# Kernel tuning notes

Measured on AMD Instinct MI355X. Metric: run time of the kernel, lower is better.

The kernel has to match this reference:

```python
import jax, jax.numpy as jnp
import numpy as np

B, S, V, E, H, NL, DFF = 16, 16, 64, 64, 8, 4, 2048
L = S * V
DH = E // H
NUM_GRIDS = 100
POI_DIM = 8
OV_DIM = 8


def setup_inputs() -> dict:
    key = jax.random.key(0)
    ks = jax.random.split(key, 32)
    sc = 0.05
    inp = {}
    inp['features'] = jax.random.normal(ks[0], (B, S, V, 3), jnp.float32)
    inp['overlap_tag'] = jax.random.randint(ks[1], (B, S, V), 0, 3)
    inp['poi_id'] = jax.random.randint(ks[2], (B, S, V), 0, NUM_GRIDS + 1)
    # embedders
    inp['W_raw'] = jax.random.normal(ks[3], (3, E), jnp.float32) * sc
    inp['b_raw'] = jnp.zeros((E,), jnp.float32)
    inp['pos_tab'] = jax.random.normal(ks[4], (S, E), jnp.float32) * sc
    inp['type_tab'] = jax.random.normal(ks[5], (V, E), jnp.float32) * sc
    inp['poi_tab'] = jax.random.normal(ks[6], (NUM_GRIDS + 1, POI_DIM), jnp.float32) * sc
    inp['overlap_tab'] = jax.random.normal(ks[7], (3, OV_DIM), jnp.float32) * sc
    inp['W_comb'] = jax.random.normal(ks[8], (E + OV_DIM + POI_DIM, E), jnp.float32) * sc
    inp['b_comb'] = jnp.zeros((E,), jnp.float32)
    # transformer layers (stacked over NL)
    inp['Wqkv'] = jax.random.normal(ks[9], (NL, E, 3 * E), jnp.float32) * sc
    inp['bqkv'] = jnp.zeros((NL, 3 * E), jnp.float32)
    inp['Wo'] = jax.random.normal(ks[10], (NL, E, E), jnp.float32) * sc
    inp['bo'] = jnp.zeros((NL, E), jnp.float32)
    inp['ln1_s'] = jnp.ones((NL, E), jnp.float32)
    inp['ln1_b'] = jnp.zeros((NL, E), jnp.float32)
    inp['W1'] = jax.random.normal(ks[11], (NL, E, DFF), jnp.float32) * sc
    inp['b1'] = jnp.zeros((NL, DFF), jnp.float32)
    inp['W2'] = jax.random.normal(ks[12], (NL, DFF, E), jnp.float32) * sc
    inp['b2'] = jnp.zeros((NL, E), jnp.float32)
    inp['ln2_s'] = jnp.ones((NL, E), jnp.float32)
    inp['ln2_b'] = jnp.zeros((NL, E), jnp.float32)
    inp['W_head'] = jax.random.normal(ks[13], (E, 3), jnp.float32) * sc
    inp['b_head'] = jnp.zeros((3,), jnp.float32)
    return inp


def _layer_norm(x, s, b):
    m = x.mean(-1, keepdims=True)
    v = ((x - m) ** 2).mean(-1, keepdims=True)
    return (x - m) / jnp.sqrt(v + 1e-5) * s + b


def _forward(features, overlap_tag, poi_id, W_raw, b_raw, pos_tab, type_tab,
             poi_tab, overlap_tab, W_comb, b_comb, Wqkv, bqkv, Wo, bo,
             ln1_s, ln1_b, W1, b1, W2, b2, ln2_s, ln2_b, W_head, b_head):
    # padding_idx=0 rows are zero (as in nn.Embedding(padding_idx=0))
    poi_tab = poi_tab.at[0].set(0.0)
    overlap_tab = overlap_tab.at[0].set(0.0)

    zero_mask = (features.sum(-1) == 0).reshape(B, L)  # [B, L]
    ov_idx = jnp.maximum(overlap_tag, 0)
    poi_idx = jnp.maximum(poi_id, 0)

    feat_e = features @ W_raw + b_raw                    # [B,S,V,E]
    concat = jnp.concatenate([feat_e, overlap_tab[ov_idx], poi_tab[poi_idx]], axis=-1)
    x = (concat @ W_comb + b_comb).reshape(B, L, E)      # [B,L,E]

    t_idx = jnp.repeat(jnp.arange(S), V)                 # [L]
    v_idx = jnp.tile(jnp.arange(V), S)                   # [L]
    struct_mask = (t_idx[:, None] != t_idx[None, :]) & (v_idx[:, None] != v_idx[None, :])
    full_mask = struct_mask[None] | zero_mask[:, None, :] | zero_mask[:, :, None]  # [B,L,L]
    bias = jnp.where(full_mask, -jnp.inf, 0.0)[:, None, :, :]  # [B,1,L,L]

    x = x + pos_tab[t_idx][None] + type_tab[v_idx][None]

    scale = 1.0 / jnp.sqrt(jnp.asarray(DH, x.dtype))
    for l in range(NL):
        qkv = x @ Wqkv[l] + bqkv[l]                      # [B,L,3E]
        q, k, v = jnp.split(qkv, 3, axis=-1)
        q = q.reshape(B, L, H, DH)
        k = k.reshape(B, L, H, DH)
        v = v.reshape(B, L, H, DH)
        scores = jnp.einsum('bqhd,bkhd->bhqk', q, k) * scale + bias
        attn = jax.nn.softmax(scores, axis=-1)
        o = jnp.einsum('bhqk,bkhd->bqhd', attn, v).reshape(B, L, E)
        x = _layer_norm(x + o @ Wo[l] + bo[l], ln1_s[l], ln1_b[l])
        ff = jax.nn.relu(x @ W1[l] + b1[l]) @ W2[l] + b2[l]
        x = _layer_norm(x + ff, ln2_s[l], ln2_b[l])

    last = x.reshape(B, S, V, E)[:, -1]                  # [B,V,E]
    return last @ W_head + b_head                        # [B,V,3]


def reference(features, overlap_tag, poi_id, W_raw, b_raw, pos_tab, type_tab,
              poi_tab, overlap_tab, W_comb, b_comb, Wqkv, bqkv, Wo, bo,
              ln1_s, ln1_b, W1, b1, W2, b2, ln2_s, ln2_b, W_head, b_head):
    return _forward(features, overlap_tag, poi_id, W_raw, b_raw, pos_tab, type_tab,
                    poi_tab, overlap_tab, W_comb, b_comb, Wqkv, bqkv, Wo, bo,
                    ln1_s, ln1_b, W1, b1, W2, b2, ln2_s, ln2_b, W_head, b_head)
```

## Files before the change

kernel.cpp:

```cpp
#include <hip/hip_runtime.h>
#include <math.h>

#define BB 16
#define SS 16
#define VVV 64
#define EE 64
#define HHH 8
#define NLAYER 4
#define DFF_ 2048
#define LL 1024
#define BL 16384
#define PERL 131072

typedef __attribute__((ext_vector_type(8))) _Float16 half8;
typedef __attribute__((ext_vector_type(4))) _Float16 half4v;
typedef __attribute__((ext_vector_type(2))) _Float16 half2v;
typedef __attribute__((ext_vector_type(4))) float f32x4;

#if defined(__has_builtin)
#if __has_builtin(__builtin_amdgcn_fdot2)
#define HAVE_FDOT2 1
#endif
#endif

#define SW64(m, k)  (((m) << 6) + ((((k) >> 3) ^ ((m) & 7)) << 3) + ((k) & 7))


__device__ __forceinline__ void ffn_load2(
    const _Float16* __restrict__ w1f, const _Float16* __restrict__ w2f, int g,
    half8 (&a1)[2][2], half8 (&b2w)[2][2], int wn, int lane)
{
  const _Float16* w1t_ = w1f + (size_t)g * 4096;
  const _Float16* w2t_ = w2f + (size_t)g * 4096;
#pragma unroll
  for (int ht = 0; ht < 2; ht++)
#pragma unroll
    for (int ks = 0; ks < 2; ks++)
      a1[ht][ks] = *(const half8*)&w1t_[(size_t)(((wn * 2 + ht) * 2 + ks) * 512) +
                                        lane * 8];
#pragma unroll
  for (int nt = 0; nt < 2; nt++)
#pragma unroll
    for (int ks = 0; ks < 2; ks++)
      b2w[nt][ks] = *(const half8*)&w2t_[(size_t)(((wn * 2 + nt) * 2 + ks) * 512) +
                                         lane * 8];
}

__device__ __forceinline__ void ffn_step2(
    const half8 (&a1)[2][2], const half8 (&b2w)[2][2], const half8 (&xb)[2][2],
    _Float16* hsbuf, const float* __restrict__ b1, int g, f32x4 (&acc)[2][2],
    int wn, int lane)
{
  int quad = lane >> 4, l15 = lane & 15;
  f32x4 hacc[2][2];
#pragma unroll
  for (int ht = 0; ht < 2; ht++)
#pragma unroll
    for (int mt = 0; mt < 2; mt++) hacc[ht][mt] = (f32x4){0.f, 0.f, 0.f, 0.f};
#pragma unroll
  for (int ks = 0; ks < 2; ks++)
#pragma unroll
    for (int ht = 0; ht < 2; ht++)
#pragma unroll
      for (int mt = 0; mt < 2; mt++)
        hacc[ht][mt] = __builtin_amdgcn_mfma_f32_16x16x32_f16(
            a1[ht][ks], xb[mt][ks], hacc[ht][mt], 0, 0, 0);
#pragma unroll
  for (int ht = 0; ht < 2; ht++) {
    float4 bb = *(const float4*)&b1[g * 64 + wn * 32 + ht * 16 + quad * 4];
#pragma unroll
    for (int mt = 0; mt < 2; mt++) {
      f32x4 hv = hacc[ht][mt];
      half4v hp = (half4v){
          (_Float16)fmaxf(hv[0] + bb.x, 0.f), (_Float16)fmaxf(hv[1] + bb.y, 0.f),
          (_Float16)fmaxf(hv[2] + bb.z, 0.f), (_Float16)fmaxf(hv[3] + bb.w, 0.f)};
      *(half4v*)&hsbuf[SW64(mt * 16 + l15, wn * 32 + ht * 16 + quad * 4)] = hp;
    }
  }
  __syncthreads();
#pragma unroll
  for (int ks = 0; ks < 2; ks++)
#pragma unroll
    for (int mt = 0; mt < 2; mt++) {
      half8 a2 = *(const half8*)&hsbuf[SW64(mt * 16 + l15, ks * 32 + quad * 8)];
#pragma unroll
      for (int nt = 0; nt < 2; nt++)
        acc[mt][nt] = __builtin_amdgcn_mfma_f32_16x16x32_f16(a2, b2w[nt][ks],
                                                             acc[mt][nt], 0, 0, 0);
    }
}

__global__ __launch_bounds__(256) void k_prepemb(
    const float* __restrict__ W1, const float* __restrict__ W2,
    const float* __restrict__ Wqkv, const float* __restrict__ Wo,
    const float* __restrict__ Wcomb,
    _Float16* __restrict__ w1f, _Float16* __restrict__ w2f,
    _Float16* __restrict__ wqkvf, _Float16* __restrict__ wof,
    const float* __restrict__ features, const int* __restrict__ ovtag,
    const int* __restrict__ poiid, const float* __restrict__ W_raw,
    const float* __restrict__ b_raw, const float* __restrict__ ov_tab,
    const float* __restrict__ poi_tab, const float* __restrict__ b_comb,
    const float* __restrict__ pos_tab, const float* __restrict__ type_tab,
    _Float16* __restrict__ x1h, float* __restrict__ zm,
    const float* __restrict__ bqkv, _Float16* __restrict__ qbuf,
    _Float16* __restrict__ kbuf, _Float16* __restrict__ vbuf)
{
  int gbx = blockIdx.x;
  int tid = threadIdx.x;

  if (gbx < 272) {
    __shared__ float t[64 * 65];
    int bx = gbx;
    int cc = tid & 63, rr = tid >> 6;
    const float* src; _Float16* dst; int astr;
    if (bx < 128) {
      int l = bx >> 5, g = bx & 31;
      src = W1 + (size_t)l * PERL + g * 64; astr = 2048;
      dst = w1f + (size_t)(l * 32 + g) * 4096;
    } else if (bx < 256) {
      int j = bx - 128; int l = j >> 5, g = j & 31;
      src = W2 + (size_t)l * PERL + (size_t)g * 64 * 64; astr = 64;
      dst = w2f + (size_t)(l * 32 + g) * 4096;
    } else if (bx < 268) {
      int j = bx - 256; int l = j / 3, g = j % 3;
      src = Wqkv + (size_t)l * 64 * 192 + g * 64; astr = 192;
      dst = wqkvf + (size_t)(l * 3 + g) * 4096;
    } else {
      int l = bx - 268;
      src = Wo + (size_t)l * 4096; astr = 64;
      dst = wof + (size_t)l * 4096;
    }
#pragma unroll
    for (int i = 0; i < 16; i++) {
      int a = i * 4 + rr;
      t[cc * 65 + a] = src[(size_t)a * astr + cc];
    }
    __syncthreads();
#pragma unroll
    for (int it = 0; it < 2; it++) {
      int c = tid + it * 256;
      int frag = c >> 6, lane = c & 63;
      int m = (frag >> 1) * 16 + (lane & 15);
      int k0 = (frag & 1) * 32 + (lane >> 4) * 8;
      const float* tr = &t[m * 65 + k0];
      half8 h;
#pragma unroll
      for (int j = 0; j < 8; j++) h[j] = (_Float16)tr[j];
      *(half8*)&dst[(size_t)c * 8] = h;
    }
    return;
  }

  constexpr int KP = 104;
  __shared__ _Float16 As[64 * KP];
  __shared__ _Float16 Bs[64 * KP];
  __shared__ _Float16 xs[4096];
  int raw = gbx - 272;
  int bx = ((raw & 7) << 5) + (raw >> 3);
  int m0 = bx * 64;
  int wave = tid >> 6, lane = tid & 63, quad = lane >> 4, l15 = lane & 15;
  int wm = wave >> 1, wn = wave & 1;
  for (int p = tid; p < 1536; p += 256) {
    int r = p / 24, s = p - r * 24; int c = s * 4;
    int row = m0 + r;
    float f0 = features[row * 3 + 0];
    float f1 = features[row * 3 + 1];
    float f2 = features[row * 3 + 2];
    if (s == 0) zm[row] = ((f0 + f1 + f2) == 0.f) ? 1.f : 0.f;
    half4v h;
#pragma unroll
    for (int j = 0; j < 4; j++) {
      int cc = c + j; float v;
      if (cc < 64) {
        v = b_raw[cc] + f0 * W_raw[cc] + f1 * W_raw[64 + cc] + f2 * W_raw[128 + cc];
      } else if (cc < 72) {
        int tt = ovtag[row]; v = (tt <= 0) ? 0.f : ov_tab[tt * 8 + cc - 64];
      } else if (cc < 80) {
        int tt = poiid[row]; v = (tt <= 0) ? 0.f : poi_tab[tt * 8 + cc - 72];
      } else v = 0.f;
      h[j] = (_Float16)v;
    }
    *(half4v*)&As[r * KP + c] = h;
  }
  for (int p = tid; p < 1536; p += 256) {
    int r = p / 24, s = p - r * 24; int c = s * 4;
    half4v h = (half4v){0, 0, 0, 0};
#pragma unroll
    for (int j = 0; j < 4; j++)
      if (c + j < 80) h[j] = (_Float16)Wcomb[(size_t)(c + j) * 64 + r];
    *(half4v*)&Bs[r * KP + c] = h;
  }
  __syncthreads();
  f32x4 acc[2][2];
#pragma unroll
  for (int mt = 0; mt < 2; mt++)
#pragma unroll
    for (int nt = 0; nt < 2; nt++) {
      float bv = b_comb[wn * 32 + nt * 16 + l15];
      acc[mt][nt] = (f32x4){bv, bv, bv, bv};
    }
#pragma unroll
  for (int ks = 0; ks < 3; ks++) {
    half8 af[2], bf[2];
#pragma unroll
    for (int mt = 0; mt < 2; mt++)
      af[mt] = *(const half8*)&As[(wm * 32 + mt * 16 + l15) * KP + ks * 32 + quad * 8];
#pragma unroll
    for (int nt = 0; nt < 2; nt++)
      bf[nt] = *(const half8*)&Bs[(wn * 32 + nt * 16 + l15) * KP + ks * 32 + quad * 8];
#pragma unroll
    for (int mt = 0; mt < 2; mt++)
#pragma unroll
      for (int nt = 0; nt < 2; nt++)
        acc[mt][nt] = __builtin_amdgcn_mfma_f32_16x16x32_f16(af[mt], bf[nt],
                                                             acc[mt][nt], 0, 0, 0);
  }
#pragma unroll
  for (int mt = 0; mt < 2; mt++)
#pragma unroll
    for (int nt = 0; nt < 2; nt++)
#pragma unroll
      for (int r = 0; r < 4; r++) {
        int lrow = wm * 32 + mt * 16 + quad * 4 + r;
        int row = m0 + lrow;
        int col = wn * 32 + nt * 16 + l15;
        int l = row & (LL - 1);
        float v = acc[mt][nt][r] +
            pos_tab[(l >> 6) * 64 + col] + type_tab[(l & 63) * 64 + col];
        x1h[(size_t)row * 64 + col] = (_Float16)v;
        xs[SW64(lrow, col)] = (_Float16)v;
      }
  __syncthreads();
  half8 af[2][2];
#pragma unroll
  for (int mt = 0; mt < 2; mt++)
#pragma unroll
    for (int ks = 0; ks < 2; ks++)
      af[mt][ks] = *(const half8*)&xs[SW64(wm * 32 + mt * 16 + l15,
                                           ks * 32 + quad * 8)];
#pragma unroll
  for (int nb = 0; nb < 3; nb++) {
    half8 bf[2][2];
#pragma unroll
    for (int nt = 0; nt < 2; nt++)
#pragma unroll
      for (int ks = 0; ks < 2; ks++) {
        int n = nb * 64 + (wn * 2 + nt) * 16 + l15;
#pragma unroll
        for (int j = 0; j < 8; j++)
          bf[nt][ks][j] =
              (_Float16)Wqkv[(size_t)(ks * 32 + quad * 8 + j) * 192 + n];
      }
    f32x4 qacc[2][2];
#pragma unroll
    for (int mt = 0; mt < 2; mt++)
#pragma unroll
      for (int nt = 0; nt < 2; nt++) {
        float bv = bqkv[nb * 64 + wn * 32 + nt * 16 + l15];
        qacc[mt][nt] = (f32x4){bv, bv, bv, bv};
      }
#pragma unroll
    for (int ks = 0; ks < 2; ks++)
#pragma unroll
      for (int mt = 0; mt < 2; mt++)
#pragma unroll
        for (int nt = 0; nt < 2; nt++)
          qacc[mt][nt] = __builtin_amdgcn_mfma_f32_16x16x32_f16(
              af[mt][ks], bf[nt][ks], qacc[mt][nt], 0, 0, 0);
    _Float16* dst = (nb == 0) ? qbuf : ((nb == 1) ? kbuf : vbuf);
#pragma unroll
    for (int mt = 0; mt < 2; mt++)
#pragma unroll
      for (int nt = 0; nt < 2; nt++) {
        int col = wn * 32 + nt * 16 + l15;
        int h = col >> 3, d = col & 7;
#pragma unroll
        for (int r = 0; r < 4; r++) {
          int row = m0 + wm * 32 + mt * 16 + quad * 4 + r;
          int b = row >> 10, rb = row & 1023;
          dst[((size_t)(b * 8 + h) * 1024 + rb) * 8 + d] = (_Float16)qacc[mt][nt][r];
        }
      }
  }
}

__global__ __launch_bounds__(256, 2) void k_layerf(
    const _Float16* __restrict__ qin, const _Float16* __restrict__ kin,
    const _Float16* __restrict__ vin, const float* __restrict__ zm,
    const _Float16* __restrict__ wof, const float* __restrict__ bo,
    _Float16* __restrict__ x1h,
    const float* __restrict__ ln1_s, const float* __restrict__ ln1_b,
    const _Float16* __restrict__ w1f, const _Float16* __restrict__ w2f,
    const float* __restrict__ b1, const float* __restrict__ b2,
    const float* __restrict__ ln2_s, const float* __restrict__ ln2_b,
    const _Float16* __restrict__ wqkvf, const float* __restrict__ bqkv,
    _Float16* __restrict__ qout, _Float16* __restrict__ kout,
    _Float16* __restrict__ vout, int doqkv,
    const float* __restrict__ Wh, const float* __restrict__ bh,
    float* __restrict__ out)
{
  __shared__ float ots[32 * 68];
  __shared__ __align__(16) _Float16 xs[2048];
  __shared__ float x2f[2048];
  __shared__ __align__(16) _Float16 hs[4][2048];
  __shared__ __align__(16) _Float16 os[2048];
  __shared__ float zsh[1024];
  __shared__ __align__(16) _Float16 kvs[8192];
  __shared__ float ots2[32 * 68];
  int tid = threadIdx.x;
  int raw = blockIdx.x;
  int bx = ((raw & 7) << 6) + (raw >> 3);
  int r0 = bx * 32;
  int rb0 = r0 & 1023;
  int wave = tid >> 6, lane = tid & 63;
  int quad = lane >> 4, l15 = lane & 15;
  int grp = wave >> 1, wn = wave & 1;
  int b = r0 >> 10;
  int tq0 = rb0 >> 6;

  for (int p = tid; p < 1024; p += 256)
    zsh[p] = (zm[b * LL + p] != 0.f) ? -20000.f : 0.f;
  for (int p = tid; p < 512; p += 256) {
    int h = p >> 6, row = p & 63;
    size_t gidx = ((size_t)(b * 8 + h) * 1024 + tq0 * 64 + row) * 8;
    *(half8*)&kvs[h * 512 + row * 8] = *(const half8*)&kin[gidx];
    *(half8*)&kvs[4096 + h * 512 + row * 8] = *(const half8*)&vin[gidx];
  }

  half8 obf[2][2];
#pragma unroll
  for (int nt = 0; nt < 2; nt++)
#pragma unroll
    for (int ks = 0; ks < 2; ks++)
      obf[nt][ks] = *(const half8*)&wof[(size_t)(((wn * 2 + nt) * 2 + ks) * 512) +
                                        lane * 8];
  float x1pre[8];
#pragma unroll
  for (int i = 0; i < 8; i++)
    x1pre[i] = (float)x1h[(size_t)(r0 + wave * 8 + i) * 64 + lane];
  float ln1sv = ln1_s[lane], ln1bv = ln1_b[lane];
  float ln2sv = ln2_s[lane], ln2bv = ln2_b[lane];
  half8 a1x[2][2], b2x[2][2], a1y[2][2], b2y[2][2];
  ffn_load2(w1f, w2f, grp, a1x, b2x, wn, lane);
  __syncthreads();

  {
    int lr = tid & 31, hh = tid >> 5;
    int rb = rb0 + lr;
    int vq = rb & 63;
    const _Float16* kb = kin + (size_t)(b * 8 + hh) * 8192;
    const _Float16* vb = vin + (size_t)(b * 8 + hh) * 8192;
    half8 qh = *(const half8*)&qin[(size_t)(b * 8 + hh) * 8192 + (size_t)rb * 8];
    const float scale = 0.3535533905932738f;
    float m = -10000.f, lsum = 0.f;
    float acc[8] = {0.f, 0.f, 0.f, 0.f, 0.f, 0.f, 0.f, 0.f};
    bool zmq = (zsh[rb] < -1.f);

    auto dot = [&](half8 kk) -> float {
      float s = 0.f;
#ifdef HAVE_FDOT2
#pragma unroll
      for (int j = 0; j < 4; j++) {
        half2v qa = (half2v){qh[2 * j], qh[2 * j + 1]};
        half2v ka = (half2v){kk[2 * j], kk[2 * j + 1]};
        s = __builtin_amdgcn_fdot2(qa, ka, s, false);
      }
#else
#pragma unroll
      for (int j = 0; j < 8; j++) s += (float)qh[j] * (float)kk[j];
#endif
      return s;
    };
    auto update = [&](float s, half8 vv) {
      float nm = fmaxf(m, s);
      float r = __expf(m - nm);
      float p = __expf(s - nm);
      lsum = lsum * r + p;
#pragma unroll
      for (int d = 0; d < 8; d++) acc[d] = acc[d] * r + p * (float)vv[d];
      m = nm;
    };

    if (!zmq) {
      for (int base = 0; base < 64; base += 4) {
        half8 kk[4], vv[4]; float sv[4];
#pragma unroll
        for (int j = 0; j < 4; j++) {
          kk[j] = *(const half8*)&kvs[hh * 512 + (base + j) * 8];
          vv[j] = *(const half8*)&kvs[4096 + hh * 512 + (base + j) * 8];
        }
#pragma unroll
        for (int j = 0; j < 4; j++)
          sv[j] = dot(kk[j]) * scale + zsh[tq0 * 64 + base + j];
#pragma unroll
        for (int j = 0; j < 4; j++) update(sv[j], vv[j]);
      }
      for (int bb = 0; bb < 5; bb++) {
        half8 kk[3], vv[3]; float sv[3];
#pragma unroll
        for (int j = 0; j < 3; j++) {
          int cc = bb * 3 + j;
          int tt = cc + ((cc >= tq0) ? 1 : 0);
          int k = tt * 64 + vq;
          kk[j] = *(const half8*)&kb[(size_t)k * 8];
          vv[j] = *(const half8*)&vb[(size_t)k * 8];
          sv[j] = zsh[k];
        }
#pragma unroll
        for (int j = 0; j < 3; j++) sv[j] += dot(kk[j]) * scale;
#pragma unroll
        for (int j = 0; j < 3; j++) update(sv[j], vv[j]);
      }
    }
    float inv = (lsum > 0.f) ? 1.f / lsum : 0.f;
    half8 o;
#pragma unroll
    for (int d = 0; d < 8; d++) o[d] = (_Float16)(acc[d] * inv);
    *(half8*)&os[SW64(lr, hh * 8)] = o;
  }
  __syncthreads();

  {
    half8 af[2];
#pragma unroll
    for (int ks = 0; ks < 2; ks++)
      af[ks] = *(const half8*)&os[SW64(grp * 16 + l15, ks * 32 + quad * 8)];
    f32x4 acc[2];
#pragma unroll
    for (int nt = 0; nt < 2; nt++) {
      float bv = bo[wn * 32 + nt * 16 + l15];
      acc[nt] = (f32x4){bv, bv, bv, bv};
    }
#pragma unroll
    for (int ks = 0; ks < 2; ks++)
#pragma unroll
      for (int nt = 0; nt < 2; nt++)
        acc[nt] = __builtin_amdgcn_mfma_f32_16x16x32_f16(af[ks], obf[nt][ks],
                                                         acc[nt], 0, 0, 0);
#pragma unroll
    for (int nt = 0; nt < 2; nt++)
#pragma unroll
      for (int r = 0; r < 4; r++)
        ots[(grp * 16 + quad * 4 + r) * 68 + wn * 32 + nt * 16 + l15] = acc[nt][r];
  }
  __syncthreads();
  for (int i = 0; i < 8; i++) {
    int row = wave * 8 + i;
    float val = ots[row * 68 + lane] + x1pre[i];
    float sum = val;
#pragma unroll
    for (int o = 32; o > 0; o >>= 1) sum += __shfl_xor(sum, o);
    float mean = sum * (1.f / 64.f);
    float d = val - mean;
    float sq = d * d;
#pragma unroll
    for (int o = 32; o > 0; o >>= 1) sq += __shfl_xor(sq, o);
    float xv = d * rsqrtf(sq * (1.f / 64.f) + 1e-5f) * ln1sv + ln1bv;
    x2f[row * 64 + lane] = xv;
    xs[SW64(row, lane)] = (_Float16)xv;
  }
  __syncthreads();

  half8 xb[2][2];
#pragma unroll
  for (int mt = 0; mt < 2; mt++)
#pragma unroll
    for (int ks = 0; ks < 2; ks++)
      xb[mt][ks] = *(const half8*)&xs[SW64(mt * 16 + l15, ks * 32 + quad * 8)];
  f32x4 acc[2][2];
#pragma unroll
  for (int mt = 0; mt < 2; mt++)
#pragma unroll
    for (int nt = 0; nt < 2; nt++) {
      float bv = (grp == 0) ? b2[wn * 32 + nt * 16 + l15] : 0.f;
      acc[mt][nt] = (f32x4){bv, bv, bv, bv};
    }
  for (int ii = 0; ii < 8; ii++) {
    ffn_load2(w1f, w2f, ii * 4 + 2 + grp, a1y, b2y, wn, lane);
    ffn_step2(a1x, b2x, xb, &hs[grp][0], b1, ii * 4 + grp, acc, wn, lane);
    if (ii < 7) ffn_load2(w1f, w2f, ii * 4 + 4 + grp, a1x, b2x, wn, lane);
    ffn_step2(a1y, b2y, xb, &hs[grp + 2][0], b1, ii * 4 + 2 + grp, acc, wn, lane);
  }
  __syncthreads();
  if (grp == 0) {
#pragma unroll
    for (int mt = 0; mt < 2; mt++)
#pragma unroll
      for (int nt = 0; nt < 2; nt++)
#pragma unroll
        for (int r = 0; r < 4; r++)
          ots[(mt * 16 + quad * 4 + r) * 68 + wn * 32 + nt * 16 + l15] =
              acc[mt][nt][r];
  }
  __syncthreads();
  if (grp == 1) {
#pragma unroll
    for (int mt = 0; mt < 2; mt++)
#pragma unroll
      for (int nt = 0; nt < 2; nt++)
#pragma unroll
        for (int r = 0; r < 4; r++)
          ots[(mt * 16 + quad * 4 + r) * 68 + wn * 32 + nt * 16 + l15] +=
              acc[mt][nt][r];
  }
  __syncthreads();
  for (int i = 0; i < 8; i++) {
    int row = wave * 8 + i;
    size_t off = (size_t)(r0 + row) * 64 + lane;
    float val = ots[row * 68 + lane] + x2f[row * 64 + lane];
    float sum = val;
#pragma unroll
    for (int o = 32; o > 0; o >>= 1) sum += __shfl_xor(sum, o);
    float mean = sum * (1.f / 64.f);
    float d = val - mean;
    float sq = d * d;
#pragma unroll
    for (int o = 32; o > 0; o >>= 1) sq += __shfl_xor(sq, o);
    float xv = d * rsqrtf(sq * (1.f / 64.f) + 1e-5f) * ln2sv + ln2bv;
    if (doqkv) x1h[off] = (_Float16)xv;
    x2f[row * 64 + lane] = xv;
    xs[SW64(row, lane)] = (_Float16)xv;
  }
  if (!doqkv) {
    __syncthreads();
    if ((bx & 31) >= 30 && tid < 96) {
      int bb2 = bx >> 5;
      int i = tid / 3, j = tid - i * 3;
      int vglob = (bx & 1) * 32 + i;
      float a = bh[j];
      for (int e = 0; e < 64; e++)
        a += x2f[i * 64 + e] * Wh[e * 3 + j];
      out[((size_t)(bb2 * 64 + vglob)) * 3 + j] = a;
    }
    return;
  }
  __syncthreads();
  half8 af[2][2];
#pragma unroll
  for (int mt = 0; mt < 2; mt++)
#pragma unroll
    for (int ks = 0; ks < 2; ks++)
      af[mt][ks] = *(const half8*)&xs[SW64(mt * 16 + l15, ks * 32 + quad * 8)];
  for (int nb = 0; nb < 3; nb++) {
    const _Float16* bt = wqkvf + (size_t)nb * 4096;
    half8 bf[2];
#pragma unroll
    for (int ks = 0; ks < 2; ks++)
      bf[ks] = *(const half8*)&bt[(size_t)((wave * 2 + ks) * 512) + lane * 8];
    f32x4 qacc[2];
#pragma unroll
    for (int mt = 0; mt < 2; mt++) {
      float bv = bqkv[nb * 64 + wave * 16 + l15];
      qacc[mt] = (f32x4){bv, bv, bv, bv};
    }
#pragma unroll
    for (int ks = 0; ks < 2; ks++)
#pragma unroll
      for (int mt = 0; mt < 2; mt++)
        qacc[mt] = __builtin_amdgcn_mfma_f32_16x16x32_f16(af[mt][ks], bf[ks],
                                                          qacc[mt], 0, 0, 0);
    _Float16* dst = (nb == 0) ? qout : ((nb == 1) ? kout : vout);
    int col = wave * 16 + l15;
    int h2 = col >> 3, d2 = col & 7;
#pragma unroll
    for (int mt = 0; mt < 2; mt++)
#pragma unroll
      for (int r = 0; r < 4; r++) {
        int row = r0 + mt * 16 + quad * 4 + r;
        int rbq = row & 1023;
        dst[((size_t)(b * 8 + h2) * 1024 + rbq) * 8 + d2] = (_Float16)qacc[mt][r];
      }
  }
}

extern "C" void kernel_launch(void* const* d_in, const int* in_sizes, int n_in,
                              void* d_out, int out_size, void* d_ws, size_t ws_size,
                              hipStream_t stream) {
  const float* features = (const float*)d_in[0];
  const int*   ovtag    = (const int*)d_in[1];
  const int*   poiid    = (const int*)d_in[2];
  const float* W_raw    = (const float*)d_in[3];
  const float* b_raw    = (const float*)d_in[4];
  const float* pos_tab  = (const float*)d_in[5];
  const float* type_tab = (const float*)d_in[6];
  const float* poi_tab  = (const float*)d_in[7];
  const float* ov_tab   = (const float*)d_in[8];
  const float* W_comb   = (const float*)d_in[9];
  const float* b_comb   = (const float*)d_in[10];
  const float* Wqkv     = (const float*)d_in[11];
  const float* bqkv     = (const float*)d_in[12];
  const float* Wo       = (const float*)d_in[13];
  const float* bo       = (const float*)d_in[14];
  const float* ln1_s    = (const float*)d_in[15];
  const float* ln1_b    = (const float*)d_in[16];
  const float* W1       = (const float*)d_in[17];
  const float* b1       = (const float*)d_in[18];
  const float* W2       = (const float*)d_in[19];
  const float* b2       = (const float*)d_in[20];
  const float* ln2_s    = (const float*)d_in[21];
  const float* ln2_b    = (const float*)d_in[22];
  const float* W_head   = (const float*)d_in[23];
  const float* b_head   = (const float*)d_in[24];
  float* out = (float*)d_out;
  float* ws  = (float*)d_ws;

  float* zm  = ws;
  _Float16* x1h = (_Float16*)(zm + BL);
  _Float16* qbA = x1h + (size_t)BL * 64;
  _Float16* kbA = qbA + (size_t)BL * 64;
  _Float16* vbA = kbA + (size_t)BL * 64;
  _Float16* qbB = vbA + (size_t)BL * 64;
  _Float16* kbB = qbB + (size_t)BL * 64;
  _Float16* vbB = kbB + (size_t)BL * 64;
  _Float16* w1f    = vbB + (size_t)BL * 64;
  _Float16* w2f    = w1f + (size_t)NLAYER * PERL;
  _Float16* wqkvf  = w2f + (size_t)NLAYER * PERL;
  _Float16* wof    = wqkvf + (size_t)NLAYER * 3 * 4096;

  k_prepemb<<<528, 256, 0, stream>>>(W1, W2, Wqkv, Wo, W_comb,
                                     w1f, w2f, wqkvf, wof,
                                     features, ovtag, poiid, W_raw, b_raw,
                                     ov_tab, poi_tab, b_comb, pos_tab, type_tab,
                                     x1h, zm, bqkv, qbA, kbA, vbA);
  for (int l = 0; l < NLAYER; l++) {
    const _Float16* qin = (l & 1) ? qbB : qbA;
    const _Float16* kin = (l & 1) ? kbB : kbA;
    const _Float16* vin = (l & 1) ? vbB : vbA;
    _Float16* qout = (l & 1) ? qbA : qbB;
    _Float16* kout = (l & 1) ? kbA : kbB;
    _Float16* vout = (l & 1) ? vbA : vbB;
    int doqkv = (l < NLAYER - 1);
    k_layerf<<<512, 256, 0, stream>>>(
        qin, kin, vin, zm,
        wof + (size_t)l * 4096, bo + l * EE, x1h,
        ln1_s + l * EE, ln1_b + l * EE,
        w1f + (size_t)l * PERL, w2f + (size_t)l * PERL,
        b1 + l * DFF_, b2 + l * EE,
        ln2_s + l * EE, ln2_b + l * EE,
        wqkvf + (size_t)(l + 1 < NLAYER ? l + 1 : 0) * 3 * 4096,
        bqkv + (l + 1 < NLAYER ? l + 1 : 0) * 192,
        qout, kout, vout, doqkv, W_head, b_head, out);
  }
}
```

Before: 273.5 us.

## Process 64 rows per block with 512 threads to halve FFN weight traffic

Each layer block now covers 64 rows (a full time step of vertices) with 8 waves instead of 32 rows with 4 waves, launching 256 blocks instead of 512. Each streamed W1/W2 chunk is applied to twice as many rows, so per-row weight traffic drops, and the K/V tile of the current time step is shared across all its vertices. The shared buffers are packed into one aliased 126 KB array, and FFN partial sums are reduced through two buffers across four wave groups. In exchange only one block fits per CU, the grid shrinks to 256 blocks, and register pressure rises from the larger accumulator tiles.

```diff
diff --git a/kernel.cpp b/kernel.cpp
--- a/kernel.cpp
+++ b/kernel.cpp
@@ -25,7 +25,6 @@
 
 #define SW64(m, k)  (((m) << 6) + ((((k) >> 3) ^ ((m) & 7)) << 3) + ((k) & 7))
 
-
 __device__ __forceinline__ void ffn_load2(
     const _Float16* __restrict__ w1f, const _Float16* __restrict__ w2f, int g,
     half8 (&a1)[2][2], half8 (&b2w)[2][2], int wn, int lane)
@@ -46,31 +45,27 @@
                                          lane * 8];
 }
 
-__device__ __forceinline__ void ffn_step2(
-    const half8 (&a1)[2][2], const half8 (&b2w)[2][2], const half8 (&xb)[2][2],
-    _Float16* hsbuf, const float* __restrict__ b1, int g, f32x4 (&acc)[2][2],
+__device__ __forceinline__ void ffn_step4(
+    const half8 (&a1)[2][2], const half8 (&b2w)[2][2], const half8 (&xb)[4][2],
+    _Float16* hsbuf, const float* __restrict__ b1, int g, f32x4 (&acc)[4][2],
     int wn, int lane)
 {
   int quad = lane >> 4, l15 = lane & 15;
-  f32x4 hacc[2][2];
-#pragma unroll
-  for (int ht = 0; ht < 2; ht++)
-#pragma unroll
-    for (int mt = 0; mt < 2; mt++) hacc[ht][mt] = (f32x4){0.f, 0.f, 0.f, 0.f};
-#pragma unroll
-  for (int ks = 0; ks < 2; ks++)
-#pragma unroll
-    for (int ht = 0; ht < 2; ht++)
-#pragma unroll
-      for (int mt = 0; mt < 2; mt++)
-        hacc[ht][mt] = __builtin_amdgcn_mfma_f32_16x16x32_f16(
-            a1[ht][ks], xb[mt][ks], hacc[ht][mt], 0, 0, 0);
 #pragma unroll
   for (int ht = 0; ht < 2; ht++) {
+    f32x4 hacc[4];
+#pragma unroll
+    for (int mt = 0; mt < 4; mt++) hacc[mt] = (f32x4){0.f, 0.f, 0.f, 0.f};
+#pragma unroll
+    for (int ks = 0; ks < 2; ks++)
+#pragma unroll
+      for (int mt = 0; mt < 4; mt++)
+        hacc[mt] = __builtin_amdgcn_mfma_f32_16x16x32_f16(
+            a1[ht][ks], xb[mt][ks], hacc[mt], 0, 0, 0);
     float4 bb = *(const float4*)&b1[g * 64 + wn * 32 + ht * 16 + quad * 4];
 #pragma unroll
-    for (int mt = 0; mt < 2; mt++) {
-      f32x4 hv = hacc[ht][mt];
+    for (int mt = 0; mt < 4; mt++) {
+      f32x4 hv = hacc[mt];
       half4v hp = (half4v){
           (_Float16)fmaxf(hv[0] + bb.x, 0.f), (_Float16)fmaxf(hv[1] + bb.y, 0.f),
           (_Float16)fmaxf(hv[2] + bb.z, 0.f), (_Float16)fmaxf(hv[3] + bb.w, 0.f)};
@@ -81,7 +76,7 @@
 #pragma unroll
   for (int ks = 0; ks < 2; ks++)
 #pragma unroll
-    for (int mt = 0; mt < 2; mt++) {
+    for (int mt = 0; mt < 4; mt++) {
       half8 a2 = *(const half8*)&hsbuf[SW64(mt * 16 + l15, ks * 32 + quad * 8)];
 #pragma unroll
       for (int nt = 0; nt < 2; nt++)
@@ -284,7 +279,7 @@
   }
 }
 
-__global__ __launch_bounds__(256, 2) void k_layerf(
+__global__ __launch_bounds__(512, 1) void k_layerf(
     const _Float16* __restrict__ qin, const _Float16* __restrict__ kin,
     const _Float16* __restrict__ vin, const float* __restrict__ zm,
     const _Float16* __restrict__ wof, const float* __restrict__ bo,
@@ -299,29 +294,30 @@
     const float* __restrict__ Wh, const float* __restrict__ bh,
     float* __restrict__ out)
 {
-  __shared__ float ots[32 * 68];
-  __shared__ __align__(16) _Float16 xs[2048];
-  __shared__ float x2f[2048];
-  __shared__ __align__(16) _Float16 hs[4][2048];
-  __shared__ __align__(16) _Float16 os[2048];
-  __shared__ float zsh[1024];
-  __shared__ __align__(16) _Float16 kvs[8192];
-  __shared__ float ots2[32 * 68];
+  __shared__ __align__(16) char smem[129024];
+  float*    ots  = (float*)smem;
+  float*    ots2 = (float*)(smem + 17408);
+  _Float16* xs   = (_Float16*)(smem + 34816);
+  float*    x2f  = (float*)(smem + 43008);
+  _Float16* hs   = (_Float16*)(smem + 59392);
+  float*    zsh  = (float*)(smem + 124928);
+  _Float16* os   = (_Float16*)(smem + 59392);
+  _Float16* kvs  = (_Float16*)(smem + 59392 + 8192);
   int tid = threadIdx.x;
   int raw = blockIdx.x;
-  int bx = ((raw & 7) << 6) + (raw >> 3);
-  int r0 = bx * 32;
+  int bx = ((raw & 7) << 5) + (raw >> 3);
+  int r0 = bx * 64;
   int rb0 = r0 & 1023;
   int wave = tid >> 6, lane = tid & 63;
   int quad = lane >> 4, l15 = lane & 15;
   int grp = wave >> 1, wn = wave & 1;
   int b = r0 >> 10;
-  int tq0 = rb0 >> 6;
-
-  for (int p = tid; p < 1024; p += 256)
+  int tq0 = bx & 15;
+
+  for (int p = tid; p < 1024; p += 512)
     zsh[p] = (zm[b * LL + p] != 0.f) ? -20000.f : 0.f;
-  for (int p = tid; p < 512; p += 256) {
-    int h = p >> 6, row = p & 63;
+  {
+    int h = tid >> 6, row = tid & 63;
     size_t gidx = ((size_t)(b * 8 + h) * 1024 + tq0 * 64 + row) * 8;
     *(half8*)&kvs[h * 512 + row * 8] = *(const half8*)&kin[gidx];
     *(half8*)&kvs[4096 + h * 512 + row * 8] = *(const half8*)&vin[gidx];
@@ -345,9 +341,8 @@
   __syncthreads();
 
   {
-    int lr = tid & 31, hh = tid >> 5;
+    int lr = tid & 63, hh = tid >> 6;
     int rb = rb0 + lr;
-    int vq = rb & 63;
     const _Float16* kb = kin + (size_t)(b * 8 + hh) * 8192;
     const _Float16* vb = vin + (size_t)(b * 8 + hh) * 8192;
     half8 qh = *(const half8*)&qin[(size_t)(b * 8 + hh) * 8192 + (size_t)rb * 8];
@@ -401,7 +396,7 @@
         for (int j = 0; j < 3; j++) {
           int cc = bb * 3 + j;
           int tt = cc + ((cc >= tq0) ? 1 : 0);
-          int k = tt * 64 + vq;
+          int k = tt * 64 + lr;
           kk[j] = *(const half8*)&kb[(size_t)k * 8];
           vv[j] = *(const half8*)&vb[(size_t)k * 8];
           sv[j] = zsh[k];
@@ -421,10 +416,11 @@
   __syncthreads();
 
   {
+    int mt_g = wave >> 1;
     half8 af[2];
 #pragma unroll
     for (int ks = 0; ks < 2; ks++)
-      af[ks] = *(const half8*)&os[SW64(grp * 16 + l15, ks * 32 + quad * 8)];
+      af[ks] = *(const half8*)&os[SW64(mt_g * 16 + l15, ks * 32 + quad * 8)];
     f32x4 acc[2];
 #pragma unroll
     for (int nt = 0; nt < 2; nt++) {
@@ -441,7 +437,7 @@
     for (int nt = 0; nt < 2; nt++)
 #pragma unroll
       for (int r = 0; r < 4; r++)
-        ots[(grp * 16 + quad * 4 + r) * 68 + wn * 32 + nt * 16 + l15] = acc[nt][r];
+        ots[(mt_g * 16 + quad * 4 + r) * 68 + wn * 32 + nt * 16 + l15] = acc[nt][r];
   }
   __syncthreads();
   for (int i = 0; i < 8; i++) {
@@ -461,53 +457,58 @@
   }
   __syncthreads();
 
-  half8 xb[2][2];
-#pragma unroll
-  for (int mt = 0; mt < 2; mt++)
+  half8 xb[4][2];
+#pragma unroll
+  for (int mt = 0; mt < 4; mt++)
 #pragma unroll
     for (int ks = 0; ks < 2; ks++)
       xb[mt][ks] = *(const half8*)&xs[SW64(mt * 16 + l15, ks * 32 + quad * 8)];
-  f32x4 acc[2][2];
-#pragma unroll
-  for (int mt = 0; mt < 2; mt++)
+  f32x4 acc[4][2];
+#pragma unroll
+  for (int mt = 0; mt < 4; mt++)
 #pragma unroll
     for (int nt = 0; nt < 2; nt++) {
       float bv = (grp == 0) ? b2[wn * 32 + nt * 16 + l15] : 0.f;
       acc[mt][nt] = (f32x4){bv, bv, bv, bv};
     }
-  for (int ii = 0; ii < 8; ii++) {
-    ffn_load2(w1f, w2f, ii * 4 + 2 + grp, a1y, b2y, wn, lane);
-    ffn_step2(a1x, b2x, xb, &hs[grp][0], b1, ii * 4 + grp, acc, wn, lane);
-    if (ii < 7) ffn_load2(w1f, w2f, ii * 4 + 4 + grp, a1x, b2x, wn, lane);
-    ffn_step2(a1y, b2y, xb, &hs[grp + 2][0], b1, ii * 4 + 2 + grp, acc, wn, lane);
-  }
-  __syncthreads();
-  if (grp == 0) {
-#pragma unroll
-    for (int mt = 0; mt < 2; mt++)
+  for (int ii = 0; ii < 4; ii++) {
+    ffn_load2(w1f, w2f, ii * 8 + 4 + grp, a1y, b2y, wn, lane);
+    ffn_step4(a1x, b2x, xb, &hs[(size_t)grp * 4096], b1, ii * 8 + grp, acc, wn,
+              lane);
+    if (ii < 3) ffn_load2(w1f, w2f, ii * 8 + 8 + grp, a1x, b2x, wn, lane);
+    ffn_step4(a1y, b2y, xb, &hs[(size_t)(grp + 4) * 4096], b1, ii * 8 + 4 + grp,
+              acc, wn, lane);
+  }
+  __syncthreads();
+  if (grp < 2) {
+    float* dst = (grp == 0) ? ots : ots2;
+#pragma unroll
+    for (int mt = 0; mt < 4; mt++)
 #pragma unroll
       for (int nt = 0; nt < 2; nt++)
 #pragma unroll
         for (int r = 0; r < 4; r++)
-          ots[(mt * 16 + quad * 4 + r) * 68 + wn * 32 + nt * 16 + l15] =
+          dst[(mt * 16 + quad * 4 + r) * 68 + wn * 32 + nt * 16 + l15] =
               acc[mt][nt][r];
   }
   __syncthreads();
-  if (grp == 1) {
-#pragma unroll
-    for (int mt = 0; mt < 2; mt++)
+  if (grp >= 2) {
+    float* dst = (grp == 2) ? ots : ots2;
+#pragma unroll
+    for (int mt = 0; mt < 4; mt++)
 #pragma unroll
       for (int nt = 0; nt < 2; nt++)
 #pragma unroll
         for (int r = 0; r < 4; r++)
-          ots[(mt * 16 + quad * 4 + r) * 68 + wn * 32 + nt * 16 + l15] +=
+          dst[(mt * 16 + quad * 4 + r) * 68 + wn * 32 + nt * 16 + l15] +=
               acc[mt][nt][r];
   }
   __syncthreads();
   for (int i = 0; i < 8; i++) {
     int row = wave * 8 + i;
     size_t off = (size_t)(r0 + row) * 64 + lane;
-    float val = ots[row * 68 + lane] + x2f[row * 64 + lane];
+    float val = ots[row * 68 + lane] + ots2[row * 68 + lane] +
+                x2f[row * 64 + lane];
     float sum = val;
 #pragma unroll
     for (int o = 32; o > 0; o >>= 1) sum += __shfl_xor(sum, o);
@@ -523,53 +524,56 @@
   }
   if (!doqkv) {
     __syncthreads();
-    if ((bx & 31) >= 30 && tid < 96) {
-      int bb2 = bx >> 5;
+    if ((bx & 15) == 15 && tid < 192) {
+      int bb2 = bx >> 4;
       int i = tid / 3, j = tid - i * 3;
-      int vglob = (bx & 1) * 32 + i;
       float a = bh[j];
       for (int e = 0; e < 64; e++)
         a += x2f[i * 64 + e] * Wh[e * 3 + j];
-      out[((size_t)(bb2 * 64 + vglob)) * 3 + j] = a;
+      out[((size_t)(bb2 * 64 + i)) * 3 + j] = a;
     }
     return;
   }
   __syncthreads();
-  half8 af[2][2];
-#pragma unroll
-  for (int mt = 0; mt < 2; mt++)
-#pragma unroll
-    for (int ks = 0; ks < 2; ks++)
-      af[mt][ks] = *(const half8*)&xs[SW64(mt * 16 + l15, ks * 32 + quad * 8)];
-  for (int nb = 0; nb < 3; nb++) {
-    const _Float16* bt = wqkvf + (size_t)nb * 4096;
-    half8 bf[2];
-#pragma unroll
-    for (int ks = 0; ks < 2; ks++)
-      bf[ks] = *(const half8*)&bt[(size_t)((wave * 2 + ks) * 512) + lane * 8];
-    f32x4 qacc[2];
-#pragma unroll
-    for (int mt = 0; mt < 2; mt++) {
-      float bv = bqkv[nb * 64 + wave * 16 + l15];
-      qacc[mt] = (f32x4){bv, bv, bv, bv};
-    }
-#pragma unroll
-    for (int ks = 0; ks < 2; ks++)
+  {
+    int mh = wave >> 2, ntile = wave & 3;
+    half8 af[2][2];
+#pragma unroll
+    for (int mt = 0; mt < 2; mt++)
+#pragma unroll
+      for (int ks = 0; ks < 2; ks++)
+        af[mt][ks] = *(const half8*)&xs[SW64(mh * 32 + mt * 16 + l15,
+                                             ks * 32 + quad * 8)];
+    for (int nb = 0; nb < 3; nb++) {
+      const _Float16* bt = wqkvf + (size_t)nb * 4096;
+      half8 bf[2];
+#pragma unroll
+      for (int ks = 0; ks < 2; ks++)
+        bf[ks] = *(const half8*)&bt[(size_t)((ntile * 2 + ks) * 512) + lane * 8];
+      f32x4 qacc[2];
+#pragma unroll
+      for (int mt = 0; mt < 2; mt++) {
+        float bv = bqkv[nb * 64 + ntile * 16 + l15];
+        qacc[mt] = (f32x4){bv, bv, bv, bv};
+      }
+#pragma unroll
+      for (int ks = 0; ks < 2; ks++)
+#pragma unroll
+        for (int mt = 0; mt < 2; mt++)
+          qacc[mt] = __builtin_amdgcn_mfma_f32_16x16x32_f16(af[mt][ks], bf[ks],
+                                                            qacc[mt], 0, 0, 0);
+      _Float16* dst = (nb == 0) ? qout : ((nb == 1) ? kout : vout);
+      int col = ntile * 16 + l15;
+      int h2 = col >> 3, d2 = col & 7;
 #pragma unroll
       for (int mt = 0; mt < 2; mt++)
-        qacc[mt] = __builtin_amdgcn_mfma_f32_16x16x32_f16(af[mt][ks], bf[ks],
-                                                          qacc[mt], 0, 0, 0);
-    _Float16* dst = (nb == 0) ? qout : ((nb == 1) ? kout : vout);
-    int col = wave * 16 + l15;
-    int h2 = col >> 3, d2 = col & 7;
-#pragma unroll
-    for (int mt = 0; mt < 2; mt++)
-#pragma unroll
-      for (int r = 0; r < 4; r++) {
-        int row = r0 + mt * 16 + quad * 4 + r;
-        int rbq = row & 1023;
-        dst[((size_t)(b * 8 + h2) * 1024 + rbq) * 8 + d2] = (_Float16)qacc[mt][r];
-      }
+#pragma unroll
+        for (int r = 0; r < 4; r++) {
+          int row = r0 + mh * 32 + mt * 16 + quad * 4 + r;
+          int rbq = row & 1023;
+          dst[((size_t)(b * 8 + h2) * 1024 + rbq) * 8 + d2] = (_Float16)qacc[mt][r];
+        }
+    }
   }
 }
 
@@ -630,7 +634,7 @@
     _Float16* kout = (l & 1) ? kbA : kbB;
     _Float16* vout = (l & 1) ? vbA : vbB;
     int doqkv = (l < NLAYER - 1);
-    k_layerf<<<512, 256, 0, stream>>>(
+    k_layerf<<<256, 512, 0, stream>>>(
         qin, kin, vin, zm,
         wof + (size_t)l * 4096, bo + l * EE, x1h,
         ln1_s + l * EE, ln1_b + l * EE,
```

New measurement: 264.1 us. -3.4%, faster.
